# Performance work log

Hardware: AMD Instinct MI355X
Metric: run time of the kernel (lower is better)

The kernel has to match this reference:

```python
import jax, jax.numpy as jnp
import numpy as np

N = 50000      # num_nodes
E = 800000     # edges (before self loops)
IN = 64        # in_dim
H = 128        # hidden_node_dim
DH = 256       # decoder_and_message_hidden_dim
L = 3          # propagation_steps


def _lin(key, fan_in, fan_out):
    s = 1.0 / np.sqrt(fan_in)
    return jax.random.uniform(key, (fan_in, fan_out), jnp.float32, -s, s)


def setup_inputs() -> dict:
    key = jax.random.key(0)
    ks = iter(jax.random.split(key, 40))
    x = jax.random.normal(next(ks), (N, IN), jnp.float32)
    edge_index = jax.random.randint(next(ks), (2, E), 0, N, jnp.int64)
    enc_W = _lin(next(ks), IN, H); enc_b = jnp.zeros((H,), jnp.float32)
    # message MLP: Linear(2H->DH) tanh, Linear(DH->DH) tanh, Linear(DH->H)
    msg_W0 = jnp.stack([_lin(next(ks), 2 * H, DH) for _ in range(L)])
    msg_b0 = jnp.zeros((L, DH), jnp.float32)
    msg_W1 = jnp.stack([_lin(next(ks), DH, DH) for _ in range(L)])
    msg_b1 = jnp.zeros((L, DH), jnp.float32)
    msg_W2 = jnp.stack([_lin(next(ks), DH, H) for _ in range(L)])
    msg_b2 = jnp.zeros((L, H), jnp.float32)
    # GRUCell params, torch layout [3H, H] chunks (r, z, n)
    gru_Wih = jnp.stack([_lin(next(ks), H, 3 * H).T for _ in range(L)])
    gru_Whh = jnp.stack([_lin(next(ks), H, 3 * H).T for _ in range(L)])
    gru_bih = jnp.zeros((L, 3 * H), jnp.float32)
    gru_bhh = jnp.zeros((L, 3 * H), jnp.float32)
    # decoder: Linear(H->DH) tanh, Linear(DH->DH) tanh, Linear(DH->1)
    dec_W0 = _lin(next(ks), H, DH); dec_b0 = jnp.zeros((DH,), jnp.float32)
    dec_W1 = _lin(next(ks), DH, DH); dec_b1 = jnp.zeros((DH,), jnp.float32)
    dec_W2 = _lin(next(ks), DH, 1); dec_b2 = jnp.zeros((1,), jnp.float32)
    return dict(x=x, edge_index=edge_index, enc_W=enc_W, enc_b=enc_b,
                msg_W0=msg_W0, msg_b0=msg_b0, msg_W1=msg_W1, msg_b1=msg_b1,
                msg_W2=msg_W2, msg_b2=msg_b2, gru_Wih=gru_Wih, gru_Whh=gru_Whh,
                gru_bih=gru_bih, gru_bhh=gru_bhh, dec_W0=dec_W0, dec_b0=dec_b0,
                dec_W1=dec_W1, dec_b1=dec_b1, dec_W2=dec_W2, dec_b2=dec_b2)


def reference(x, edge_index, enc_W, enc_b, msg_W0, msg_b0, msg_W1, msg_b1,
              msg_W2, msg_b2, gru_Wih, gru_Whh, gru_bih, gru_bhh,
              dec_W0, dec_b0, dec_W1, dec_b1, dec_W2, dec_b2):
    n = x.shape[0]
    # add self loops (PyG add_self_loops appends (v, v))
    loops = jnp.arange(n, dtype=edge_index.dtype)
    src = jnp.concatenate([edge_index[0], loops])  # j (source)
    dst = jnp.concatenate([edge_index[1], loops])  # i (target)
    counts = jax.ops.segment_sum(jnp.ones_like(dst, jnp.float32), dst, num_segments=n)
    h = jnp.tanh(x @ enc_W + enc_b)                # encoder [N, H]
    for l in range(L):
        # message: f([x_i || x_j]) per edge
        m = jnp.concatenate([h[dst], h[src]], axis=-1)            # [E+N, 2H]
        m = jnp.tanh(m @ msg_W0[l] + msg_b0[l])
        m = jnp.tanh(m @ msg_W1[l] + msg_b1[l])
        m = m @ msg_W2[l] + msg_b2[l]                              # [E+N, H]
        aggr = jax.ops.segment_sum(m, dst, num_segments=n) / counts[:, None]
        # GRUCell(input=aggr, hidden=h)
        gi = aggr @ gru_Wih[l].T + gru_bih[l]                      # [N, 3H]
        gh = h @ gru_Whh[l].T + gru_bhh[l]
        i_r, i_z, i_n = jnp.split(gi, 3, axis=-1)
        h_r, h_z, h_n = jnp.split(gh, 3, axis=-1)
        r = jax.nn.sigmoid(i_r + h_r)
        z = jax.nn.sigmoid(i_z + h_z)
        nn_ = jnp.tanh(i_n + r * h_n)
        h = (1.0 - z) * nn_ + z * h
    # decoder
    y = jnp.tanh(h @ dec_W0 + dec_b0)
    y = jnp.tanh(y @ dec_W1 + dec_b1)
    y = y @ dec_W2 + dec_b2                                        # [N, 1]
    return y.reshape(-1, n)[0]                                     # view(-1, N).squeeze(0)
```

## Files before the change

### kernel.cpp

```cpp
#include <hip/hip_runtime.h>

typedef __bf16 bf16x8 __attribute__((ext_vector_type(8)));
typedef float  f32x4  __attribute__((ext_vector_type(4)));

__device__ inline unsigned short f2bf(float f){
  __bf16 b = (__bf16)f;
  return __builtin_bit_cast(unsigned short, b);
}
__device__ inline unsigned int pack2bf(float lo, float hi){
  return (unsigned)f2bf(lo) | ((unsigned)f2bf(hi) << 16);
}
__device__ inline float tanh_fast(float x){
  float e = __builtin_amdgcn_exp2f(x * 2.8853900817779268f);
  return 1.0f - 2.0f * __builtin_amdgcn_rcpf(e + 1.0f);
}
__device__ inline float sigmoid_fast(float x){
  float e = __builtin_amdgcn_exp2f(x * -1.4426950408889634f);
  return __builtin_amdgcn_rcpf(1.0f + e);
}
__device__ inline float bflo(unsigned int u){ return __uint_as_float(u << 16); }
__device__ inline float bfhi(unsigned int u){ return __uint_as_float(u & 0xffff0000u); }

__global__ void k_count(const int* __restrict__ ei, int* __restrict__ cnt, int E){
  int e = blockIdx.x * 256 + threadIdx.x;
  if (e < E) atomicAdd(&cnt[ei[E + e]], 1);
}

__global__ __launch_bounds__(1024) void k_scan(const int* __restrict__ cnt, int* __restrict__ cursor, int N){
  __shared__ int partial[1024];
  int t = threadIdx.x;
  int chunk = (N + 1023) / 1024;
  int lo = t * chunk, hi = min(lo + chunk, N);
  int s = 0;
  for (int v = lo; v < hi; v++) s += cnt[v] + 1;
  partial[t] = s;
  __syncthreads();
  for (int off = 1; off < 1024; off <<= 1){
    int val = (t >= off) ? partial[t - off] : 0;
    __syncthreads();
    partial[t] += val;
    __syncthreads();
  }
  int base = (t == 0) ? 0 : partial[t - 1];
  for (int v = lo; v < hi; v++){ cursor[v] = base; base += cnt[v] + 1; }
}

__global__ void k_scatter(const int* __restrict__ ei, int* __restrict__ cursor,
                          int* __restrict__ srcS, int* __restrict__ dstS, int E, int N){
  int i = blockIdx.x * 256 + threadIdx.x;
  int Et = E + N;
  if (i >= Et) return;
  int s, d;
  if (i < E){ s = ei[i]; d = ei[E + i]; } else { s = d = i - E; }
  int pos = atomicAdd(&cursor[d], 1);
// ... 161 lines not shown
    }
    bf16x8 afA[4], afB[4];
    #pragma unroll
    for (int ct = 0; ct < 4; ct++){
      int r = c64 + ct * 16 + l15;
      afA[ct] = *(const bf16x8*)(wa + (size_t)r * 256 + koff);
      afB[ct] = *(const bf16x8*)(wb + (size_t)r * 256 + koff);
    }
    #pragma unroll
    for (int ct = 0; ct < 4; ct++)
      #pragma unroll
      for (int nt = 0; nt < 4; nt++){
        accA[ct][nt] = __builtin_amdgcn_mfma_f32_16x16x32_bf16(afA[ct], bfr[nt], accA[ct][nt], 0, 0, 0);
        accB[ct][nt] = __builtin_amdgcn_mfma_f32_16x16x32_bf16(afB[ct], bfr[nt], accB[ct][nt], 0, 0, 0);
      }
  }
  #pragma unroll
  for (int ct = 0; ct < 4; ct++){
    int c = c64 + ct * 16 + kg * 4;
    #pragma unroll
    for (int nt = 0; nt < 4; nt++){
      int node = n0 + nt * 16 + l15;
      if (node >= N) continue;
      f32x4 va = accA[ct][nt], vb = accB[ct][nt];
      uint2 oa, ob;
      oa.x = pack2bf(va[0], va[1]); oa.y = pack2bf(va[2], va[3]);
      ob.x = pack2bf(vb[0], vb[1]); ob.y = pack2bf(vb[2], vb[3]);
      *(uint2*)(A + (size_t)node * 256 + c) = oa;
      *(uint2*)(B + (size_t)node * 256 + c) = ob;
    }
  }
}

__global__ __launch_bounds__(256, 3) void k_edge(
        const int* __restrict__ srcS, const int* __restrict__ dstS,
        const unsigned short* __restrict__ Abuf, const unsigned short* __restrict__ Bbuf,
        const unsigned short* __restrict__ W1T, const unsigned short* __restrict__ W2T,
        const float* __restrict__ b1, const float* __restrict__ b2,
        float* __restrict__ aggr){
  __shared__ __align__(16) unsigned char smem[64 * 512];
  __shared__ __align__(16) unsigned char t1h[64 * 256];
  __shared__ int sIdx[64], dIdx[64];
  __shared__ int segStart[64];
  __shared__ int nsegS, endAllS;
  unsigned char* t0 = smem;
  int t = threadIdx.x;
  int e0 = blockIdx.x * 64;
  if (t < 64){ sIdx[t] = srcS[e0 + t]; dIdx[t] = dstS[e0 + t]; }
  __syncthreads();

  int chunk = t & 31, rbase = t >> 5;
  uint4 av[8], bv[8];
  #pragma unroll
  for (int p = 0; p < 8; p++){
    int row = p * 8 + rbase;
    int d = dIdx[row], s = sIdx[row];
    if (d >= 0){
      av[p] = *(const uint4*)(Abuf + (size_t)d * 256 + chunk * 8);
      bv[p] = *(const uint4*)(Bbuf + (size_t)s * 256 + chunk * 8);
    } else { av[p] = make_uint4(0,0,0,0); bv[p] = make_uint4(0,0,0,0); }
  }
  if (t < 64){
    int d = dIdx[t];
    bool valid = (d >= 0);
    bool flag  = valid && (t == 0 || dIdx[t - 1] != d);
    unsigned long long startMask = __ballot(flag);
    unsigned long long invMask   = __ballot(!valid);
    if (flag){
      int s = __popcll(startMask & ((1ull << t) - 1ull));
      segStart[s] = t;
    }
    if (t == 0){
      nsegS   = (int)__popcll(startMask);
      endAllS = 64 - (int)__popcll(invMask);
    }
  }

  {
    #pragma unroll
    for (int p = 0; p < 8; p++){
      int r = p * 8 + rbase;
      unsigned int o[4]; unsigned int ua, ub;
      ua = av[p].x; ub = bv[p].x;
      o[0] = pack2bf(tanh_fast(bflo(ua)+bflo(ub)), tanh_fast(bfhi(ua)+bfhi(ub)));
      ua = av[p].y; ub = bv[p].y;
      o[1] = pack2bf(tanh_fast(bflo(ua)+bflo(ub)), tanh_fast(bfhi(ua)+bfhi(ub)));
      ua = av[p].z; ub = bv[p].z;
      o[2] = pack2bf(tanh_fast(bflo(ua)+bflo(ub)), tanh_fast(bfhi(ua)+bfhi(ub)));
      ua = av[p].w; ub = bv[p].w;
      o[3] = pack2bf(tanh_fast(bflo(ua)+bflo(ub)), tanh_fast(bfhi(ua)+bfhi(ub)));
      *(uint4*)(t0 + r * 512 + ((chunk * 16) ^ ((r & 7) << 4))) = make_uint4(o[0],o[1],o[2],o[3]);
    }
  }
  __syncthreads();

  int wv = t >> 6, lane = t & 63, l15 = lane & 15, kg = lane >> 4;
  const unsigned char* w1b = (const unsigned char*)W1T;
  const unsigned char* w2b = (const unsigned char*)W2T;
  int hbase = wv * 32;

  f32x4 acc2[2][4];
  #pragma unroll
  for (int ht = 0; ht < 2; ht++){
    int hb_ = hbase + ht * 16 + kg * 4;
    float4 c4 = *(const float4*)(b2 + hb_);
    f32x4 binit = {c4.x, c4.y, c4.z, c4.w};
    #pragma unroll
    for (int b_ = 0; b_ < 4; b_++) acc2[ht][b_] = binit;
  }

  #pragma unroll
  for (int pass = 0; pass < 2; pass++){
    {
      f32x4 acc[2][4];
      int nbase = pass * 128 + wv * 32;
      #pragma unroll
      for (int nt = 0; nt < 2; nt++){
        int ng = nbase + nt * 16 + kg * 4;
        float4 c4 = *(const float4*)(b1 + ng);
        f32x4 binit = {c4.x, c4.y, c4.z, c4.w};
        #pragma unroll
        for (int b_ = 0; b_ < 4; b_++) acc[nt][b_] = binit;
      }
      #pragma unroll
      for (int ks = 0; ks < 8; ks++){
        int koff = ks * 64 + kg * 16;
        bf16x8 afr[2], bfr[4];
        #pragma unroll
        for (int nt = 0; nt < 2; nt++)
          afr[nt] = *(const bf16x8*)(w1b + (size_t)(nbase + nt * 16 + l15) * 512 + koff);
        #pragma unroll
        for (int et = 0; et < 4; et++){
          int row = et * 16 + l15;
          bfr[et] = *(const bf16x8*)(t0 + row * 512 + (koff ^ ((row & 7) << 4)));
        }
        #pragma unroll
        for (int nt = 0; nt < 2; nt++)
          #pragma unroll
          for (int et = 0; et < 4; et++)
            acc[nt][et] = __builtin_amdgcn_mfma_f32_16x16x32_bf16(afr[nt], bfr[et], acc[nt][et], 0, 0, 0);
      }
      #pragma unroll
      for (int nt = 0; nt < 2; nt++){
        int nl2 = (wv * 32 + nt * 16 + kg * 4) * 2;
        #pragma unroll
        for (int et = 0; et < 4; et++){
          int edge = et * 16 + l15;
          f32x4 v = acc[nt][et];
          unsigned int p0 = pack2bf(tanh_fast(v[0]), tanh_fast(v[1]));
          unsigned int p1 = pack2bf(tanh_fast(v[2]), tanh_fast(v[3]));
          *(uint2*)(t1h + edge * 256 + (nl2 ^ ((edge & 7) << 4))) = make_uint2(p0, p1);
        }
      }
    }
    __syncthreads();

    #pragma unroll
    for (int ks = 0; ks < 4; ks++){
      int koff  = ks * 64 + kg * 16;
      int wkoff = pass * 256 + koff;
      bf16x8 afr[2], bfr[4];
      #pragma unroll
      for (int ht = 0; ht < 2; ht++)
        afr[ht] = *(const bf16x8*)(w2b + (size_t)(hbase + ht * 16 + l15) * 512 + wkoff);
      #pragma unroll
      for (int et = 0; et < 4; et++){
        int row = et * 16 + l15;
        bfr[et] = *(const bf16x8*)(t1h + row * 256 + (koff ^ ((row & 7) << 4)));
      }
      #pragma unroll
      for (int ht = 0; ht < 2; ht++)
        #pragma unroll
        for (int et = 0; et < 4; et++)
          acc2[ht][et] = __builtin_amdgcn_mfma_f32_16x16x32_bf16(afr[ht], bfr[et], acc2[ht][et], 0, 0, 0);
    }
    __syncthreads();
  }

  {
    #pragma unroll
    for (int ht = 0; ht < 2; ht++){
      int hb_ = hbase + ht * 16 + kg * 4;
      int cch = hb_ >> 2;
      #pragma unroll
      for (int et = 0; et < 4; et++){
        int edge = et * 16 + l15;
        f32x4 v = acc2[ht][et];
        float4 o; o.x = v[0]; o.y = v[1]; o.z = v[2]; o.w = v[3];
        *(float4*)(smem + edge * 512 + ((cch ^ (edge & 7)) << 4)) = o;
      }
    }
  }
  __syncthreads();

  {
    int c = t & 31, sstr = t >> 5;
    int nseg = nsegS, endAll = endAllS;
    for (int s = sstr; s < nseg; s += 8){
      int st = segStart[s];
      int en = (s + 1 < nseg) ? segStart[s + 1] : endAll;
      int d  = dIdx[st];
      float4 sum; sum.x = sum.y = sum.z = sum.w = 0.f;
      for (int e = st; e < en; e++){
        float4 v = *(const float4*)(smem + e * 512 + ((c ^ (e & 7)) << 4));
        sum.x += v.x; sum.y += v.y; sum.z += v.z; sum.w += v.w;
      }
      float* base = aggr + (size_t)d * 128 + c * 4;
      atomicAdd(base + 0, sum.x);
      atomicAdd(base + 1, sum.y);
      atomicAdd(base + 2, sum.z);
      atomicAdd(base + 3, sum.w);
    }
  }
}

__global__ __launch_bounds__(256) void k_gru(const float* __restrict__ aggr, const int* __restrict__ cnt,
    float* __restrict__ h, unsigned short* __restrict__ hb,
    const unsigned short* __restrict__ Wcat, const float* __restrict__ brz,
    const float* __restrict__ bin, const float* __restrict__ bhn, int N){
  __shared__ __align__(16) unsigned char u[64 * 512];
  __shared__ __align__(16) unsigned char hf[64 * 512];
  int n0 = blockIdx.x * 64, t = threadIdx.x;
  {
    int row = t >> 2, node = n0 + row;
    int q4 = t & 3;
    bool isA = q4 < 2;
    float inv = 0.f;
    if (isA && node < N) inv = __builtin_amdgcn_rcpf((float)(cnt[node] + 1));
    #pragma unroll
    for (int p = 0; p < 8; p++){
      int ch = q4 * 8 + p;
      unsigned int o[4] = {0,0,0,0};
      if (node < N){
        if (isA){
          const float* s = aggr + (size_t)node * 128 + ch * 8;
          float4 a = *(const float4*)s, b = *(const float4*)(s + 4);
          a.x *= inv; a.y *= inv; a.z *= inv; a.w *= inv;
          b.x *= inv; b.y *= inv; b.z *= inv; b.w *= inv;
          o[0] = pack2bf(a.x, a.y); o[1] = pack2bf(a.z, a.w);
          o[2] = pack2bf(b.x, b.y); o[3] = pack2bf(b.z, b.w);
        } else {
          const float* s = h + (size_t)node * 128 + (ch - 16) * 8;
          float4 a = *(const float4*)s, b = *(const float4*)(s + 4);
          o[0] = pack2bf(a.x, a.y); o[1] = pack2bf(a.z, a.w);
          o[2] = pack2bf(b.x, b.y); o[3] = pack2bf(b.z, b.w);
// ... 213 lines not shown
    if (part == 0 && (n0 + node) < N) out[n0 + node] = p + db2[0];
  }
}

extern "C" void kernel_launch(void* const* d_in, const int* in_sizes, int n_in,
                              void* d_out, int out_size, void* d_ws, size_t ws_size,
                              hipStream_t stream){
  const float* x     = (const float*)d_in[0];
  const int*   ei    = (const int*)  d_in[1];
  const float* encW  = (const float*)d_in[2];
  const float* encb  = (const float*)d_in[3];
  const float* msgW0 = (const float*)d_in[4];
  const float* msgb0 = (const float*)d_in[5];
  const float* msgW1 = (const float*)d_in[6];
  const float* msgb1 = (const float*)d_in[7];
  const float* msgW2 = (const float*)d_in[8];
  const float* msgb2 = (const float*)d_in[9];
  const float* gWih  = (const float*)d_in[10];
  const float* gWhh  = (const float*)d_in[11];
  const float* gbih  = (const float*)d_in[12];
  const float* gbhh  = (const float*)d_in[13];
  const float* dW0   = (const float*)d_in[14];
  const float* db0   = (const float*)d_in[15];
  const float* dW1   = (const float*)d_in[16];
  const float* db1   = (const float*)d_in[17];
  const float* dW2   = (const float*)d_in[18];
  const float* db2   = (const float*)d_in[19];
  int N = in_sizes[0] / 64;
  int E = in_sizes[1] / 2;
  float* out = (float*)d_out;

  int Et = E + N;
  int EtPad = (Et + 63) & ~63;

  char* ws = (char*)d_ws;
  size_t off = 0;
  auto alloc = [&](size_t bytes)->void*{
    void* p = ws + off; off += (bytes + 255) & ~(size_t)255; return p;
  };
  float*          h      = (float*)         alloc((size_t)N * 128 * 4);
  unsigned short* hbuf   = (unsigned short*)alloc((size_t)N * 128 * 2);
  unsigned short* Abuf   = (unsigned short*)alloc((size_t)N * 256 * 2);
  unsigned short* Bbuf   = (unsigned short*)alloc((size_t)N * 256 * 2);
  float*          aggr   = (float*)         alloc((size_t)N * 128 * 4);
  int*            cnt    = (int*)           alloc((size_t)N * 4);
  int*            cursor = (int*)           alloc((size_t)N * 4);
  int*            srcS   = (int*)           alloc((size_t)EtPad * 4);
  int*            dstS   = (int*)           alloc((size_t)EtPad * 4);
  unsigned short* W1T    = (unsigned short*)alloc((size_t)3 * 65536 * 2);
  unsigned short* W2T    = (unsigned short*)alloc((size_t)3 * 32768 * 2);
  unsigned short* W0T    = (unsigned short*)alloc((size_t)3 * 65536 * 2);
  unsigned short* Wcat   = (unsigned short*)alloc((size_t)3 * 98304 * 2);
  unsigned short* encWT  = (unsigned short*)alloc((size_t)8192 * 2);
  unsigned short* dW0T   = (unsigned short*)alloc((size_t)32768 * 2);
  unsigned short* dW1T   = (unsigned short*)alloc((size_t)65536 * 2);
  float*          brz    = (float*)         alloc((size_t)768 * 4);
  float*          binb   = (float*)         alloc((size_t)384 * 4);
  float*          bhnb   = (float*)         alloc((size_t)384 * 4);
  (void)ws_size; (void)n_in; (void)out_size;

  hipMemsetAsync(cnt, 0, (size_t)N * 4, stream);
  hipMemsetAsync(dstS, 0xFF, (size_t)EtPad * 4, stream);
  k_count<<<(E + 255) / 256, 256, 0, stream>>>(ei, cnt, E);
  k_scan<<<1, 1024, 0, stream>>>(cnt, cursor, N);
  k_scatter<<<(Et + 255) / 256, 256, 0, stream>>>(ei, cursor, srcS, dstS, E, N);
  k_wprep<<<(3 * 65536 + 3 * 32768 + 255) / 256, 256, 0, stream>>>(msgW1, msgW2, W1T, W2T);
  k_wprep2<<<(3 * 65536 + 255) / 256, 256, 0, stream>>>(msgW0, W0T);
  k_wprep3<<<(3 * 98304 + 255) / 256, 256, 0, stream>>>(gWih, gWhh, Wcat);
  k_wprep4<<<(108032 + 255) / 256, 256, 0, stream>>>(encW, dW0, dW1, gbih, gbhh,
                                                     encWT, dW0T, dW1T, brz, binb, bhnb);

  int nb64 = (N + 63) / 64;
  k_enc<<<nb64, 256, 0, stream>>>(x, encWT, encb, h, hbuf, N);

  int eb = EtPad / 64;
  for (int l = 0; l < 3; l++){
    k_ab<<<nb64, 256, 0, stream>>>(hbuf, W0T + (size_t)l * 65536, msgb0 + (size_t)l * 256,
                                   Abuf, Bbuf, N);
    hipMemsetAsync(aggr, 0, (size_t)N * 128 * 4, stream);
    k_edge<<<eb, 256, 0, stream>>>(srcS, dstS, Abuf, Bbuf,
        W1T + (size_t)l * 65536, W2T + (size_t)l * 32768,
        msgb1 + (size_t)l * 256, msgb2 + (size_t)l * 128,
        aggr);
    k_gru<<<nb64, 256, 0, stream>>>(aggr, cnt, h, hbuf,
        Wcat + (size_t)l * 98304, brz + (size_t)l * 256,
        binb + (size_t)l * 128, bhnb + (size_t)l * 128, N);
  }
  k_dec<<<nb64, 256, 0, stream>>>(hbuf, dW0T, db0, dW1T, db1, dW2, db2, out, N);
}
```

Baseline: 1.573 ms.

## Make edge kernel persistent with double-buffered gather prefetch across tiles

Converts k_edge from one 64-edge tile per block into a persistent kernel with 768 blocks, each walking a contiguous range of tiles. The next tile's indices and its A/B row gathers are issued before the current tile's MFMA work, so gather latency overlaps compute. It also swaps __syncthreads for a barrier that waits only on LDS counters, leaving the prefetched global loads in flight. Block-to-range mapping is interleaved by blockIdx&7, and the extra live registers for prefetch may reduce occupancy.

```diff
diff --git a/kernel.cpp b/kernel.cpp
--- a/kernel.cpp
+++ b/kernel.cpp
@@ -20,6 +20,11 @@
 }
 __device__ inline float bflo(unsigned int u){ return __uint_as_float(u << 16); }
 __device__ inline float bfhi(unsigned int u){ return __uint_as_float(u & 0xffff0000u); }
+
+__device__ __forceinline__ void bar_nodrain(){
+  asm volatile("s_waitcnt lgkmcnt(0)" ::: "memory");
+  __builtin_amdgcn_s_barrier();
+}
 
 __global__ void k_count(const int* __restrict__ ei, int* __restrict__ cnt, int E){
   int e = blockIdx.x * 256 + threadIdx.x;
@@ -252,46 +257,72 @@
         const unsigned short* __restrict__ Abuf, const unsigned short* __restrict__ Bbuf,
         const unsigned short* __restrict__ W1T, const unsigned short* __restrict__ W2T,
         const float* __restrict__ b1, const float* __restrict__ b2,
-        float* __restrict__ aggr){
+        float* __restrict__ aggr, int nT){
   __shared__ __align__(16) unsigned char smem[64 * 512];
   __shared__ __align__(16) unsigned char t1h[64 * 256];
-  __shared__ int sIdx[64], dIdx[64];
+  __shared__ int sI[2][64], dI[2][64];
   __shared__ int segStart[64];
   __shared__ int nsegS, endAllS;
   unsigned char* t0 = smem;
   int t = threadIdx.x;
-  int e0 = blockIdx.x * 64;
-  if (t < 64){ sIdx[t] = srcS[e0 + t]; dIdx[t] = dstS[e0 + t]; }
+
+  int nb   = gridDim.x;
+  int rb   = (blockIdx.x & 7) * (nb >> 3) + (blockIdx.x >> 3);
+  int cpb  = (nT + nb - 1) / nb;
+  int tstart = rb * cpb;
+  int tend   = min(tstart + cpb, nT);
+  if (tstart >= tend) return;
+
+  int chunk = t & 31, rbase = t >> 5;
+  int wv = t >> 6, lane = t & 63, l15 = lane & 15, kg = lane >> 4;
+  const unsigned char* w1b = (const unsigned char*)W1T;
+  const unsigned char* w2b = (const unsigned char*)W2T;
+  int hbase = wv * 32;
+
+  uint4 av[8], bv[8];
+  auto issue = [&](int buf){
+    #pragma unroll
+    for (int p = 0; p < 8; p++){
+      int row = p * 8 + rbase;
+      int d = dI[buf][row], s = sI[buf][row];
+      if (d >= 0){
+        av[p] = *(const uint4*)(Abuf + (size_t)d * 256 + chunk * 8);
+        bv[p] = *(const uint4*)(Bbuf + (size_t)s * 256 + chunk * 8);
+      } else { av[p] = make_uint4(0,0,0,0); bv[p] = make_uint4(0,0,0,0); }
+    }
+  };
+
+  if (t < 64){
+    int e = tstart * 64 + t;
+    sI[0][t] = srcS[e]; dI[0][t] = dstS[e];
+  }
   __syncthreads();
-
-  int chunk = t & 31, rbase = t >> 5;
-  uint4 av[8], bv[8];
-  #pragma unroll
-  for (int p = 0; p < 8; p++){
-    int row = p * 8 + rbase;
-    int d = dIdx[row], s = sIdx[row];
-    if (d >= 0){
-      av[p] = *(const uint4*)(Abuf + (size_t)d * 256 + chunk * 8);
-      bv[p] = *(const uint4*)(Bbuf + (size_t)s * 256 + chunk * 8);
-    } else { av[p] = make_uint4(0,0,0,0); bv[p] = make_uint4(0,0,0,0); }
-  }
-  if (t < 64){
-    int d = dIdx[t];
-    bool valid = (d >= 0);
-    bool flag  = valid && (t == 0 || dIdx[t - 1] != d);
-    unsigned long long startMask = __ballot(flag);
-    unsigned long long invMask   = __ballot(!valid);
-    if (flag){
-      int s = __popcll(startMask & ((1ull << t) - 1ull));
-      segStart[s] = t;
-    }
-    if (t == 0){
-      nsegS   = (int)__popcll(startMask);
-      endAllS = 64 - (int)__popcll(invMask);
-    }
-  }
-
-  {
+  issue(0);
+  int par = 0;
+
+  for (int ti = tstart; ti < tend; ++ti){
+    bool hasNext = (ti + 1 < tend);
+    int sReg = 0, dReg = -1;
+    if (hasNext && t < 64){
+      int e = (ti + 1) * 64 + t;
+      sReg = srcS[e]; dReg = dstS[e];
+    }
+    if (t < 64){
+      int d = dI[par][t];
+      bool valid = (d >= 0);
+      bool flag  = valid && (t == 0 || dI[par][t - 1] != d);
+      unsigned long long startMask = __ballot(flag);
+      unsigned long long invMask   = __ballot(!valid);
+      if (flag){
+        int s = __popcll(startMask & ((1ull << t) - 1ull));
+        segStart[s] = t;
+      }
+      if (t == 0){
+        nsegS   = (int)__popcll(startMask);
+        endAllS = 64 - (int)__popcll(invMask);
+      }
+    }
+
     #pragma unroll
     for (int p = 0; p < 8; p++){
       int r = p * 8 + rbase;
@@ -306,93 +337,89 @@
       o[3] = pack2bf(tanh_fast(bflo(ua)+bflo(ub)), tanh_fast(bfhi(ua)+bfhi(ub)));
       *(uint4*)(t0 + r * 512 + ((chunk * 16) ^ ((r & 7) << 4))) = make_uint4(o[0],o[1],o[2],o[3]);
     }
-  }
-  __syncthreads();
-
-  int wv = t >> 6, lane = t & 63, l15 = lane & 15, kg = lane >> 4;
-  const unsigned char* w1b = (const unsigned char*)W1T;
-  const unsigned char* w2b = (const unsigned char*)W2T;
-  int hbase = wv * 32;
-
-  f32x4 acc2[2][4];
-  #pragma unroll
-  for (int ht = 0; ht < 2; ht++){
-    int hb_ = hbase + ht * 16 + kg * 4;
-    float4 c4 = *(const float4*)(b2 + hb_);
-    f32x4 binit = {c4.x, c4.y, c4.z, c4.w};
-    #pragma unroll
-    for (int b_ = 0; b_ < 4; b_++) acc2[ht][b_] = binit;
-  }
-
-  #pragma unroll
-  for (int pass = 0; pass < 2; pass++){
-    {
-      f32x4 acc[2][4];
-      int nbase = pass * 128 + wv * 32;
-      #pragma unroll
-      for (int nt = 0; nt < 2; nt++){
-        int ng = nbase + nt * 16 + kg * 4;
-        float4 c4 = *(const float4*)(b1 + ng);
-        f32x4 binit = {c4.x, c4.y, c4.z, c4.w};
-        #pragma unroll
-        for (int b_ = 0; b_ < 4; b_++) acc[nt][b_] = binit;
-      }
-      #pragma unroll
-      for (int ks = 0; ks < 8; ks++){
-        int koff = ks * 64 + kg * 16;
+    if (hasNext && t < 64){ sI[par ^ 1][t] = sReg; dI[par ^ 1][t] = dReg; }
+    bar_nodrain();
+
+    if (hasNext) issue(par ^ 1);
+
+    f32x4 acc2[2][4];
+    #pragma unroll
+    for (int ht = 0; ht < 2; ht++){
+      int hb_ = hbase + ht * 16 + kg * 4;
+      float4 c4 = *(const float4*)(b2 + hb_);
+      f32x4 binit = {c4.x, c4.y, c4.z, c4.w};
+      #pragma unroll
+      for (int b_ = 0; b_ < 4; b_++) acc2[ht][b_] = binit;
+    }
+
+    #pragma unroll
+    for (int pass = 0; pass < 2; pass++){
+      {
+        f32x4 acc[2][4];
+        int nbase = pass * 128 + wv * 32;
+        #pragma unroll
+        for (int nt = 0; nt < 2; nt++){
+          int ng = nbase + nt * 16 + kg * 4;
+          float4 c4 = *(const float4*)(b1 + ng);
+          f32x4 binit = {c4.x, c4.y, c4.z, c4.w};
+          #pragma unroll
+          for (int b_ = 0; b_ < 4; b_++) acc[nt][b_] = binit;
+        }
+        #pragma unroll
+        for (int ks = 0; ks < 8; ks++){
+          int koff = ks * 64 + kg * 16;
+          bf16x8 afr[2], bfr[4];
+          #pragma unroll
+          for (int nt = 0; nt < 2; nt++)
+            afr[nt] = *(const bf16x8*)(w1b + (size_t)(nbase + nt * 16 + l15) * 512 + koff);
+          #pragma unroll
+          for (int et = 0; et < 4; et++){
+            int row = et * 16 + l15;
+            bfr[et] = *(const bf16x8*)(t0 + row * 512 + (koff ^ ((row & 7) << 4)));
+          }
+          #pragma unroll
+          for (int nt = 0; nt < 2; nt++)
+            #pragma unroll
+            for (int et = 0; et < 4; et++)
+              acc[nt][et] = __builtin_amdgcn_mfma_f32_16x16x32_bf16(afr[nt], bfr[et], acc[nt][et], 0, 0, 0);
+        }
+        #pragma unroll
+        for (int nt = 0; nt < 2; nt++){
+          int nl2 = (wv * 32 + nt * 16 + kg * 4) * 2;
+          #pragma unroll
+          for (int et = 0; et < 4; et++){
+            int edge = et * 16 + l15;
+            f32x4 v = acc[nt][et];
+            unsigned int p0 = pack2bf(tanh_fast(v[0]), tanh_fast(v[1]));
+            unsigned int p1 = pack2bf(tanh_fast(v[2]), tanh_fast(v[3]));
+            *(uint2*)(t1h + edge * 256 + (nl2 ^ ((edge & 7) << 4))) = make_uint2(p0, p1);
+          }
+        }
+      }
+      bar_nodrain();
+
+      #pragma unroll
+      for (int ks = 0; ks < 4; ks++){
+        int koff  = ks * 64 + kg * 16;
+        int wkoff = pass * 256 + koff;
         bf16x8 afr[2], bfr[4];
         #pragma unroll
-        for (int nt = 0; nt < 2; nt++)
-          afr[nt] = *(const bf16x8*)(w1b + (size_t)(nbase + nt * 16 + l15) * 512 + koff);
+        for (int ht = 0; ht < 2; ht++)
+          afr[ht] = *(const bf16x8*)(w2b + (size_t)(hbase + ht * 16 + l15) * 512 + wkoff);
         #pragma unroll
         for (int et = 0; et < 4; et++){
           int row = et * 16 + l15;
-          bfr[et] = *(const bf16x8*)(t0 + row * 512 + (koff ^ ((row & 7) << 4)));
+          bfr[et] = *(const bf16x8*)(t1h + row * 256 + (koff ^ ((row & 7) << 4)));
         }
         #pragma unroll
-        for (int nt = 0; nt < 2; nt++)
+        for (int ht = 0; ht < 2; ht++)
           #pragma unroll
           for (int et = 0; et < 4; et++)
-            acc[nt][et] = __builtin_amdgcn_mfma_f32_16x16x32_bf16(afr[nt], bfr[et], acc[nt][et], 0, 0, 0);
-      }
-      #pragma unroll
-      for (int nt = 0; nt < 2; nt++){
-        int nl2 = (wv * 32 + nt * 16 + kg * 4) * 2;
-        #pragma unroll
-        for (int et = 0; et < 4; et++){
-          int edge = et * 16 + l15;
-          f32x4 v = acc[nt][et];
-          unsigned int p0 = pack2bf(tanh_fast(v[0]), tanh_fast(v[1]));
-          unsigned int p1 = pack2bf(tanh_fast(v[2]), tanh_fast(v[3]));
-          *(uint2*)(t1h + edge * 256 + (nl2 ^ ((edge & 7) << 4))) = make_uint2(p0, p1);
-        }
-      }
-    }
-    __syncthreads();
-
-    #pragma unroll
-    for (int ks = 0; ks < 4; ks++){
-      int koff  = ks * 64 + kg * 16;
-      int wkoff = pass * 256 + koff;
-      bf16x8 afr[2], bfr[4];
-      #pragma unroll
-      for (int ht = 0; ht < 2; ht++)
-        afr[ht] = *(const bf16x8*)(w2b + (size_t)(hbase + ht * 16 + l15) * 512 + wkoff);
-      #pragma unroll
-      for (int et = 0; et < 4; et++){
-        int row = et * 16 + l15;
-        bfr[et] = *(const bf16x8*)(t1h + row * 256 + (koff ^ ((row & 7) << 4)));
-      }
-      #pragma unroll
-      for (int ht = 0; ht < 2; ht++)
-        #pragma unroll
-        for (int et = 0; et < 4; et++)
-          acc2[ht][et] = __builtin_amdgcn_mfma_f32_16x16x32_bf16(afr[ht], bfr[et], acc2[ht][et], 0, 0, 0);
-    }
-    __syncthreads();
-  }
-
-  {
+            acc2[ht][et] = __builtin_amdgcn_mfma_f32_16x16x32_bf16(afr[ht], bfr[et], acc2[ht][et], 0, 0, 0);
+      }
+      bar_nodrain();
+    }
+
     #pragma unroll
     for (int ht = 0; ht < 2; ht++){
       int hb_ = hbase + ht * 16 + kg * 4;
@@ -405,27 +432,29 @@
         *(float4*)(smem + edge * 512 + ((cch ^ (edge & 7)) << 4)) = o;
       }
     }
-  }
-  __syncthreads();
-
-  {
-    int c = t & 31, sstr = t >> 5;
-    int nseg = nsegS, endAll = endAllS;
-    for (int s = sstr; s < nseg; s += 8){
-      int st = segStart[s];
-      int en = (s + 1 < nseg) ? segStart[s + 1] : endAll;
-      int d  = dIdx[st];
-      float4 sum; sum.x = sum.y = sum.z = sum.w = 0.f;
-      for (int e = st; e < en; e++){
-        float4 v = *(const float4*)(smem + e * 512 + ((c ^ (e & 7)) << 4));
-        sum.x += v.x; sum.y += v.y; sum.z += v.z; sum.w += v.w;
-      }
-      float* base = aggr + (size_t)d * 128 + c * 4;
-      atomicAdd(base + 0, sum.x);
-      atomicAdd(base + 1, sum.y);
-      atomicAdd(base + 2, sum.z);
-      atomicAdd(base + 3, sum.w);
-    }
+    bar_nodrain();
+
+    {
+      int c = t & 31, sstr = t >> 5;
+      int nseg = nsegS, endAll = endAllS;
+      for (int s = sstr; s < nseg; s += 8){
+        int st = segStart[s];
+        int en = (s + 1 < nseg) ? segStart[s + 1] : endAll;
+        int d  = dI[par][st];
+        float4 sum; sum.x = sum.y = sum.z = sum.w = 0.f;
+        for (int e = st; e < en; e++){
+          float4 v = *(const float4*)(smem + e * 512 + ((c ^ (e & 7)) << 4));
+          sum.x += v.x; sum.y += v.y; sum.z += v.z; sum.w += v.w;
+        }
+        float* base = aggr + (size_t)d * 128 + c * 4;
+        atomicAdd(base + 0, sum.x);
+        atomicAdd(base + 1, sum.y);
+        atomicAdd(base + 2, sum.z);
+        atomicAdd(base + 3, sum.w);
+      }
+    }
+    bar_nodrain();
+    par ^= 1;
   }
 }
 
@@ -705,6 +734,7 @@
 
   int Et = E + N;
   int EtPad = (Et + 63) & ~63;
+  int nT = EtPad / 64;
 
   char* ws = (char*)d_ws;
   size_t off = 0;
@@ -746,15 +776,15 @@
   int nb64 = (N + 63) / 64;
   k_enc<<<nb64, 256, 0, stream>>>(x, encWT, encb, h, hbuf, N);
 
-  int eb = EtPad / 64;
+  const int EDGE_BLOCKS = 768;
   for (int l = 0; l < 3; l++){
     k_ab<<<nb64, 256, 0, stream>>>(hbuf, W0T + (size_t)l * 65536, msgb0 + (size_t)l * 256,
                                    Abuf, Bbuf, N);
     hipMemsetAsync(aggr, 0, (size_t)N * 128 * 4, stream);
-    k_edge<<<eb, 256, 0, stream>>>(srcS, dstS, Abuf, Bbuf,
+    k_edge<<<EDGE_BLOCKS, 256, 0, stream>>>(srcS, dstS, Abuf, Bbuf,
         W1T + (size_t)l * 65536, W2T + (size_t)l * 32768,
         msgb1 + (size_t)l * 256, msgb2 + (size_t)l * 128,
-        aggr);
+        aggr, nT);
     k_gru<<<nb64, 256, 0, stream>>>(aggr, cnt, h, hbuf,
         Wcat + (size_t)l * 98304, brz + (size_t)l * 256,
         binb + (size_t)l * 128, bhnb + (size_t)l * 128, N);
```

Measured after the change: 2.174 ms. 38.2% more time.

## Make edge-MLP kernel wave-independent with 16 edges per wave

Applied to the files above, without the earlier changes.

Restructures the edge kernel so each wavefront handles its own 16 edges end to end, with private LDS tiles. Block-wide __syncthreads barriers are replaced by per-wave LDS waitcnt fences, and segment detection moves to shuffles and ballots. Each wave now walks all 256/128 output columns, so every weight fragment is reused across only 16 edges instead of 64. That raises global and L2 weight traffic per edge in exchange for removing barriers and the cross-wave dependencies. Relying only on s_waitcnt for intra-wave LDS ordering also assumes the whole wavefront executes in lockstep.

```diff
diff --git a/kernel.cpp b/kernel.cpp
--- a/kernel.cpp
+++ b/kernel.cpp
@@ -20,6 +20,10 @@
 }
 __device__ inline float bflo(unsigned int u){ return __uint_as_float(u << 16); }
 __device__ inline float bfhi(unsigned int u){ return __uint_as_float(u & 0xffff0000u); }
+
+__device__ __forceinline__ void fence_lds(){
+  asm volatile("s_waitcnt lgkmcnt(0)" ::: "memory");
+}
 
 __global__ void k_count(const int* __restrict__ ei, int* __restrict__ cnt, int E){
   int e = blockIdx.x * 256 + threadIdx.x;
@@ -253,171 +257,140 @@
         const unsigned short* __restrict__ W1T, const unsigned short* __restrict__ W2T,
         const float* __restrict__ b1, const float* __restrict__ b2,
         float* __restrict__ aggr){
-  __shared__ __align__(16) unsigned char smem[64 * 512];
-  __shared__ __align__(16) unsigned char t1h[64 * 256];
-  __shared__ int sIdx[64], dIdx[64];
-  __shared__ int segStart[64];
-  __shared__ int nsegS, endAllS;
-  unsigned char* t0 = smem;
+  __shared__ __align__(16) unsigned char t0s[4 * 8192];
+  __shared__ __align__(16) unsigned char t1s[4 * 4096];
+  __shared__ int segStartS[4][16];
+  __shared__ int segDstS[4][16];
   int t = threadIdx.x;
-  int e0 = blockIdx.x * 64;
-  if (t < 64){ sIdx[t] = srcS[e0 + t]; dIdx[t] = dstS[e0 + t]; }
-  __syncthreads();
-
-  int chunk = t & 31, rbase = t >> 5;
+  int wv = t >> 6, lane = t & 63, l15 = lane & 15, kg = lane >> 4;
+  unsigned char* t0w = t0s + wv * 8192;
+  unsigned char* t1w = t1s + wv * 4096;
+
+  int e0 = (blockIdx.x * 4 + wv) * 16;
+  int sv = 0, dv = -1;
+  if (lane < 16){ sv = srcS[e0 + lane]; dv = dstS[e0 + lane]; }
+  int myEdge = lane >> 2;
+  int c2 = lane & 3;
+  int dE = __shfl(dv, myEdge);
+  int sE = __shfl(sv, myEdge);
+
   uint4 av[8], bv[8];
   #pragma unroll
   for (int p = 0; p < 8; p++){
-    int row = p * 8 + rbase;
-    int d = dIdx[row], s = sIdx[row];
-    if (d >= 0){
-      av[p] = *(const uint4*)(Abuf + (size_t)d * 256 + chunk * 8);
-      bv[p] = *(const uint4*)(Bbuf + (size_t)s * 256 + chunk * 8);
+    int ch = c2 * 8 + p;
+    if (dE >= 0){
+      av[p] = *(const uint4*)(Abuf + (size_t)dE * 256 + ch * 8);
+      bv[p] = *(const uint4*)(Bbuf + (size_t)sE * 256 + ch * 8);
     } else { av[p] = make_uint4(0,0,0,0); bv[p] = make_uint4(0,0,0,0); }
   }
-  if (t < 64){
-    int d = dIdx[t];
-    bool valid = (d >= 0);
-    bool flag  = valid && (t == 0 || dIdx[t - 1] != d);
-    unsigned long long startMask = __ballot(flag);
-    unsigned long long invMask   = __ballot(!valid);
-    if (flag){
-      int s = __popcll(startMask & ((1ull << t) - 1ull));
-      segStart[s] = t;
-    }
-    if (t == 0){
-      nsegS   = (int)__popcll(startMask);
-      endAllS = 64 - (int)__popcll(invMask);
-    }
-  }
-
-  {
-    #pragma unroll
-    for (int p = 0; p < 8; p++){
-      int r = p * 8 + rbase;
-      unsigned int o[4]; unsigned int ua, ub;
-      ua = av[p].x; ub = bv[p].x;
-      o[0] = pack2bf(tanh_fast(bflo(ua)+bflo(ub)), tanh_fast(bfhi(ua)+bfhi(ub)));
-      ua = av[p].y; ub = bv[p].y;
-      o[1] = pack2bf(tanh_fast(bflo(ua)+bflo(ub)), tanh_fast(bfhi(ua)+bfhi(ub)));
-      ua = av[p].z; ub = bv[p].z;
-      o[2] = pack2bf(tanh_fast(bflo(ua)+bflo(ub)), tanh_fast(bfhi(ua)+bfhi(ub)));
-      ua = av[p].w; ub = bv[p].w;
-      o[3] = pack2bf(tanh_fast(bflo(ua)+bflo(ub)), tanh_fast(bfhi(ua)+bfhi(ub)));
-      *(uint4*)(t0 + r * 512 + ((chunk * 16) ^ ((r & 7) << 4))) = make_uint4(o[0],o[1],o[2],o[3]);
-    }
-  }
-  __syncthreads();
-
-  int wv = t >> 6, lane = t & 63, l15 = lane & 15, kg = lane >> 4;
+
+  int prevd = __shfl(dv, (lane == 0) ? 0 : (lane - 1));
+  bool valid16 = (lane < 16) && (dv >= 0);
+  bool flag = valid16 && (lane == 0 || prevd != dv);
+  unsigned long long sm  = __ballot(flag);
+  unsigned long long ivm = __ballot((lane < 16) && (dv < 0));
+  int nseg   = (int)__popcll(sm);
+  int endAll = 16 - (int)__popcll(ivm);
+  if (flag){
+    int s = (int)__popcll(sm & ((1ull << lane) - 1ull));
+    segStartS[wv][s] = lane;
+    segDstS[wv][s]   = dv;
+  }
+
+  #pragma unroll
+  for (int p = 0; p < 8; p++){
+    int ch = c2 * 8 + p;
+    unsigned int o[4]; unsigned int ua, ub;
+    ua = av[p].x; ub = bv[p].x;
+    o[0] = pack2bf(tanh_fast(bflo(ua)+bflo(ub)), tanh_fast(bfhi(ua)+bfhi(ub)));
+    ua = av[p].y; ub = bv[p].y;
+    o[1] = pack2bf(tanh_fast(bflo(ua)+bflo(ub)), tanh_fast(bfhi(ua)+bfhi(ub)));
+    ua = av[p].z; ub = bv[p].z;
+    o[2] = pack2bf(tanh_fast(bflo(ua)+bflo(ub)), tanh_fast(bfhi(ua)+bfhi(ub)));
+    ua = av[p].w; ub = bv[p].w;
+    o[3] = pack2bf(tanh_fast(bflo(ua)+bflo(ub)), tanh_fast(bfhi(ua)+bfhi(ub)));
+    *(uint4*)(t0w + myEdge * 512 + ((ch * 16) ^ ((myEdge & 7) << 4))) = make_uint4(o[0],o[1],o[2],o[3]);
+  }
+  fence_lds();
+
   const unsigned char* w1b = (const unsigned char*)W1T;
   const unsigned char* w2b = (const unsigned char*)W2T;
-  int hbase = wv * 32;
-
-  f32x4 acc2[2][4];
-  #pragma unroll
-  for (int ht = 0; ht < 2; ht++){
-    int hb_ = hbase + ht * 16 + kg * 4;
+
+  f32x4 acc2[8];
+  #pragma unroll
+  for (int ht = 0; ht < 8; ht++){
+    int hb_ = ht * 16 + kg * 4;
     float4 c4 = *(const float4*)(b2 + hb_);
     f32x4 binit = {c4.x, c4.y, c4.z, c4.w};
-    #pragma unroll
-    for (int b_ = 0; b_ < 4; b_++) acc2[ht][b_] = binit;
+    acc2[ht] = binit;
   }
 
   #pragma unroll
   for (int pass = 0; pass < 2; pass++){
     {
-      f32x4 acc[2][4];
-      int nbase = pass * 128 + wv * 32;
-      #pragma unroll
-      for (int nt = 0; nt < 2; nt++){
+      f32x4 acc[8];
+      int nbase = pass * 128;
+      #pragma unroll
+      for (int nt = 0; nt < 8; nt++){
         int ng = nbase + nt * 16 + kg * 4;
         float4 c4 = *(const float4*)(b1 + ng);
         f32x4 binit = {c4.x, c4.y, c4.z, c4.w};
-        #pragma unroll
-        for (int b_ = 0; b_ < 4; b_++) acc[nt][b_] = binit;
+        acc[nt] = binit;
       }
       #pragma unroll
       for (int ks = 0; ks < 8; ks++){
         int koff = ks * 64 + kg * 16;
-        bf16x8 afr[2], bfr[4];
+        bf16x8 bfr = *(const bf16x8*)(t0w + l15 * 512 + (koff ^ ((l15 & 7) << 4)));
         #pragma unroll
-        for (int nt = 0; nt < 2; nt++)
-          afr[nt] = *(const bf16x8*)(w1b + (size_t)(nbase + nt * 16 + l15) * 512 + koff);
-        #pragma unroll
-        for (int et = 0; et < 4; et++){
-          int row = et * 16 + l15;
-          bfr[et] = *(const bf16x8*)(t0 + row * 512 + (koff ^ ((row & 7) << 4)));
+        for (int nt = 0; nt < 8; nt++){
+          bf16x8 afr = *(const bf16x8*)(w1b + (size_t)(nbase + nt * 16 + l15) * 512 + koff);
+          acc[nt] = __builtin_amdgcn_mfma_f32_16x16x32_bf16(afr, bfr, acc[nt], 0, 0, 0);
         }
-        #pragma unroll
-        for (int nt = 0; nt < 2; nt++)
-          #pragma unroll
-          for (int et = 0; et < 4; et++)
-            acc[nt][et] = __builtin_amdgcn_mfma_f32_16x16x32_bf16(afr[nt], bfr[et], acc[nt][et], 0, 0, 0);
-      }
-      #pragma unroll
-      for (int nt = 0; nt < 2; nt++){
-        int nl2 = (wv * 32 + nt * 16 + kg * 4) * 2;
-        #pragma unroll
-        for (int et = 0; et < 4; et++){
-          int edge = et * 16 + l15;
-          f32x4 v = acc[nt][et];
-          unsigned int p0 = pack2bf(tanh_fast(v[0]), tanh_fast(v[1]));
-          unsigned int p1 = pack2bf(tanh_fast(v[2]), tanh_fast(v[3]));
-          *(uint2*)(t1h + edge * 256 + (nl2 ^ ((edge & 7) << 4))) = make_uint2(p0, p1);
-        }
-      }
-    }
-    __syncthreads();
+      }
+      #pragma unroll
+      for (int nt = 0; nt < 8; nt++){
+        int nl2 = (nt * 16 + kg * 4) * 2;
+        f32x4 v = acc[nt];
+        unsigned int p0 = pack2bf(tanh_fast(v[0]), tanh_fast(v[1]));
+        unsigned int p1 = pack2bf(tanh_fast(v[2]), tanh_fast(v[3]));
+        *(uint2*)(t1w + l15 * 256 + (nl2 ^ ((l15 & 7) << 4))) = make_uint2(p0, p1);
+      }
+    }
+    fence_lds();
 
     #pragma unroll
     for (int ks = 0; ks < 4; ks++){
       int koff  = ks * 64 + kg * 16;
       int wkoff = pass * 256 + koff;
-      bf16x8 afr[2], bfr[4];
-      #pragma unroll
-      for (int ht = 0; ht < 2; ht++)
-        afr[ht] = *(const bf16x8*)(w2b + (size_t)(hbase + ht * 16 + l15) * 512 + wkoff);
-      #pragma unroll
-      for (int et = 0; et < 4; et++){
-        int row = et * 16 + l15;
-        bfr[et] = *(const bf16x8*)(t1h + row * 256 + (koff ^ ((row & 7) << 4)));
-      }
-      #pragma unroll
-      for (int ht = 0; ht < 2; ht++)
-        #pragma unroll
-        for (int et = 0; et < 4; et++)
-          acc2[ht][et] = __builtin_amdgcn_mfma_f32_16x16x32_bf16(afr[ht], bfr[et], acc2[ht][et], 0, 0, 0);
-    }
-    __syncthreads();
-  }
+      bf16x8 bfr = *(const bf16x8*)(t1w + l15 * 256 + (koff ^ ((l15 & 7) << 4)));
+      #pragma unroll
+      for (int ht = 0; ht < 8; ht++){
+        bf16x8 afr = *(const bf16x8*)(w2b + (size_t)(ht * 16 + l15) * 512 + wkoff);
+        acc2[ht] = __builtin_amdgcn_mfma_f32_16x16x32_bf16(afr, bfr, acc2[ht], 0, 0, 0);
+      }
+    }
+    fence_lds();
+  }
+
+  #pragma unroll
+  for (int ht = 0; ht < 8; ht++){
+    int hb_ = ht * 16 + kg * 4;
+    int cch = hb_ >> 2;
+    f32x4 v = acc2[ht];
+    float4 o; o.x = v[0]; o.y = v[1]; o.z = v[2]; o.w = v[3];
+    *(float4*)(t0w + l15 * 512 + ((cch ^ (l15 & 7)) << 4)) = o;
+  }
+  fence_lds();
 
   {
-    #pragma unroll
-    for (int ht = 0; ht < 2; ht++){
-      int hb_ = hbase + ht * 16 + kg * 4;
-      int cch = hb_ >> 2;
-      #pragma unroll
-      for (int et = 0; et < 4; et++){
-        int edge = et * 16 + l15;
-        f32x4 v = acc2[ht][et];
-        float4 o; o.x = v[0]; o.y = v[1]; o.z = v[2]; o.w = v[3];
-        *(float4*)(smem + edge * 512 + ((cch ^ (edge & 7)) << 4)) = o;
-      }
-    }
-  }
-  __syncthreads();
-
-  {
-    int c = t & 31, sstr = t >> 5;
-    int nseg = nsegS, endAll = endAllS;
-    for (int s = sstr; s < nseg; s += 8){
-      int st = segStart[s];
-      int en = (s + 1 < nseg) ? segStart[s + 1] : endAll;
-      int d  = dIdx[st];
+    int c = lane & 31, sstr = lane >> 5;
+    for (int s = sstr; s < nseg; s += 2){
+      int st = segStartS[wv][s];
+      int en = (s + 1 < nseg) ? segStartS[wv][s + 1] : endAll;
+      int d  = segDstS[wv][s];
       float4 sum; sum.x = sum.y = sum.z = sum.w = 0.f;
       for (int e = st; e < en; e++){
-        float4 v = *(const float4*)(smem + e * 512 + ((c ^ (e & 7)) << 4));
+        float4 v = *(const float4*)(t0w + e * 512 + ((c ^ (e & 7)) << 4));
         sum.x += v.x; sum.y += v.y; sum.z += v.z; sum.w += v.w;
       }
       float* base = aggr + (size_t)d * 128 + c * 4;
```

Result: slower. 4.389 ms (+179.0%).

## Shrink edge-kernel LDS, compute segments via wave shuffles, raise occupancy

Applied to the files above, without the earlier changes.

The edge MLP kernel now stages the second hidden layer in four quarter passes of 64 columns instead of two halves of 128. This cuts the intermediate LDS buffer to 8KB and the total to 40KB, allowing four blocks per CU instead of three. Edge indices and segment boundaries are computed per wave with shuffles and ballots instead of shared arrays, removing one barrier. Barriers now wait only on LDS counters, not global memory, so the gathers can stay in flight. The cost is more barriers per block and smaller per-pass MFMA tiles with less weight reuse.

```diff
diff --git a/kernel.cpp b/kernel.cpp
--- a/kernel.cpp
+++ b/kernel.cpp
@@ -20,6 +20,16 @@
 }
 __device__ inline float bflo(unsigned int u){ return __uint_as_float(u << 16); }
 __device__ inline float bfhi(unsigned int u){ return __uint_as_float(u & 0xffff0000u); }
+
+__device__ __forceinline__ void bar_nodrain(){
+  asm volatile("s_waitcnt lgkmcnt(0)" ::: "memory");
+  __builtin_amdgcn_s_barrier();
+}
+
+__device__ inline int nthbit(unsigned long long m, int n){
+  for (int k = 0; k < n; k++) m &= m - 1;
+  return m ? (int)__builtin_ctzll(m) : 0;
+}
 
 __global__ void k_count(const int* __restrict__ ei, int* __restrict__ cnt, int E){
   int e = blockIdx.x * 256 + threadIdx.x;
@@ -247,69 +257,67 @@
   }
 }
 
-__global__ __launch_bounds__(256, 3) void k_edge(
+__global__ __launch_bounds__(256, 4) void k_edge(
         const int* __restrict__ srcS, const int* __restrict__ dstS,
         const unsigned short* __restrict__ Abuf, const unsigned short* __restrict__ Bbuf,
         const unsigned short* __restrict__ W1T, const unsigned short* __restrict__ W2T,
         const float* __restrict__ b1, const float* __restrict__ b2,
         float* __restrict__ aggr){
-  __shared__ __align__(16) unsigned char smem[64 * 512];
-  __shared__ __align__(16) unsigned char t1h[64 * 256];
-  __shared__ int sIdx[64], dIdx[64];
-  __shared__ int segStart[64];
-  __shared__ int nsegS, endAllS;
-  unsigned char* t0 = smem;
+  __shared__ __align__(16) unsigned char lds[40960];
+  unsigned char* t0  = lds;
+  unsigned char* t1q = lds + 32768;
   int t = threadIdx.x;
+  int wv = t >> 6, lane = t & 63, l15 = lane & 15, kg = lane >> 4;
   int e0 = blockIdx.x * 64;
-  if (t < 64){ sIdx[t] = srcS[e0 + t]; dIdx[t] = dstS[e0 + t]; }
-  __syncthreads();
-
-  int chunk = t & 31, rbase = t >> 5;
+
+  int sv = srcS[e0 + lane];
+  int dv = dstS[e0 + lane];
+
+  int chunk = lane & 31;
+  int rbase = wv * 2 + (lane >> 5);
   uint4 av[8], bv[8];
   #pragma unroll
   for (int p = 0; p < 8; p++){
     int row = p * 8 + rbase;
-    int d = dIdx[row], s = sIdx[row];
+    int d = __shfl(dv, row), s = __shfl(sv, row);
     if (d >= 0){
       av[p] = *(const uint4*)(Abuf + (size_t)d * 256 + chunk * 8);
       bv[p] = *(const uint4*)(Bbuf + (size_t)s * 256 + chunk * 8);
     } else { av[p] = make_uint4(0,0,0,0); bv[p] = make_uint4(0,0,0,0); }
   }
-  if (t < 64){
-    int d = dIdx[t];
-    bool valid = (d >= 0);
-    bool flag  = valid && (t == 0 || dIdx[t - 1] != d);
-    unsigned long long startMask = __ballot(flag);
-    unsigned long long invMask   = __ballot(!valid);
-    if (flag){
-      int s = __popcll(startMask & ((1ull << t) - 1ull));
-      segStart[s] = t;
-    }
-    if (t == 0){
-      nsegS   = (int)__popcll(startMask);
-      endAllS = 64 - (int)__popcll(invMask);
-    }
-  }
-
+
+  int prevd = __shfl(dv, (lane == 0) ? 0 : (lane - 1));
+  bool valid = (dv >= 0);
+  bool flag  = valid && (lane == 0 || prevd != dv);
+  unsigned long long sm  = __ballot(flag);
+  unsigned long long ivm = __ballot(!valid);
+  int nseg   = (int)__popcll(sm);
+  int endAll = 64 - (int)__popcll(ivm);
+
+  int segSt, segEn, segD;
   {
-    #pragma unroll
-    for (int p = 0; p < 8; p++){
-      int r = p * 8 + rbase;
-      unsigned int o[4]; unsigned int ua, ub;
-      ua = av[p].x; ub = bv[p].x;
-      o[0] = pack2bf(tanh_fast(bflo(ua)+bflo(ub)), tanh_fast(bfhi(ua)+bfhi(ub)));
-      ua = av[p].y; ub = bv[p].y;
-      o[1] = pack2bf(tanh_fast(bflo(ua)+bflo(ub)), tanh_fast(bfhi(ua)+bfhi(ub)));
-      ua = av[p].z; ub = bv[p].z;
-      o[2] = pack2bf(tanh_fast(bflo(ua)+bflo(ub)), tanh_fast(bfhi(ua)+bfhi(ub)));
-      ua = av[p].w; ub = bv[p].w;
-      o[3] = pack2bf(tanh_fast(bflo(ua)+bflo(ub)), tanh_fast(bfhi(ua)+bfhi(ub)));
-      *(uint4*)(t0 + r * 512 + ((chunk * 16) ^ ((r & 7) << 4))) = make_uint4(o[0],o[1],o[2],o[3]);
-    }
-  }
-  __syncthreads();
-
-  int wv = t >> 6, lane = t & 63, l15 = lane & 15, kg = lane >> 4;
+    int st_ = nthbit(sm, lane);
+    int en_ = (lane + 1 < nseg) ? nthbit(sm, lane + 1) : endAll;
+    segSt = st_; segEn = en_;
+    segD  = __shfl(dv, st_);
+  }
+
+  #pragma unroll
+  for (int p = 0; p < 8; p++){
+    int r = p * 8 + rbase;
+    unsigned int o[4]; unsigned int ua, ub;
+    ua = av[p].x; ub = bv[p].x;
+    o[0] = pack2bf(tanh_fast(bflo(ua)+bflo(ub)), tanh_fast(bfhi(ua)+bfhi(ub)));
+    ua = av[p].y; ub = bv[p].y;
+    o[1] = pack2bf(tanh_fast(bflo(ua)+bflo(ub)), tanh_fast(bfhi(ua)+bfhi(ub)));
+    ua = av[p].z; ub = bv[p].z;
+    o[2] = pack2bf(tanh_fast(bflo(ua)+bflo(ub)), tanh_fast(bfhi(ua)+bfhi(ub)));
+    ua = av[p].w; ub = bv[p].w;
+    o[3] = pack2bf(tanh_fast(bflo(ua)+bflo(ub)), tanh_fast(bfhi(ua)+bfhi(ub)));
+    *(uint4*)(t0 + r * 512 + ((chunk * 16) ^ ((r & 7) << 4))) = make_uint4(o[0],o[1],o[2],o[3]);
+  }
+  bar_nodrain();
+
   const unsigned char* w1b = (const unsigned char*)W1T;
   const unsigned char* w2b = (const unsigned char*)W2T;
   int hbase = wv * 32;
@@ -325,55 +333,47 @@
   }
 
   #pragma unroll
-  for (int pass = 0; pass < 2; pass++){
+  for (int pass = 0; pass < 4; pass++){
     {
-      f32x4 acc[2][4];
-      int nbase = pass * 128 + wv * 32;
-      #pragma unroll
-      for (int nt = 0; nt < 2; nt++){
-        int ng = nbase + nt * 16 + kg * 4;
+      int nbase = pass * 64 + wv * 16;
+      f32x4 acc[4];
+      {
+        int ng = nbase + kg * 4;
         float4 c4 = *(const float4*)(b1 + ng);
         f32x4 binit = {c4.x, c4.y, c4.z, c4.w};
         #pragma unroll
-        for (int b_ = 0; b_ < 4; b_++) acc[nt][b_] = binit;
+        for (int b_ = 0; b_ < 4; b_++) acc[b_] = binit;
       }
       #pragma unroll
       for (int ks = 0; ks < 8; ks++){
         int koff = ks * 64 + kg * 16;
-        bf16x8 afr[2], bfr[4];
-        #pragma unroll
-        for (int nt = 0; nt < 2; nt++)
-          afr[nt] = *(const bf16x8*)(w1b + (size_t)(nbase + nt * 16 + l15) * 512 + koff);
+        bf16x8 afr = *(const bf16x8*)(w1b + (size_t)(nbase + l15) * 512 + koff);
+        bf16x8 bfr[4];
         #pragma unroll
         for (int et = 0; et < 4; et++){
           int row = et * 16 + l15;
           bfr[et] = *(const bf16x8*)(t0 + row * 512 + (koff ^ ((row & 7) << 4)));
         }
         #pragma unroll
-        for (int nt = 0; nt < 2; nt++)
-          #pragma unroll
-          for (int et = 0; et < 4; et++)
-            acc[nt][et] = __builtin_amdgcn_mfma_f32_16x16x32_bf16(afr[nt], bfr[et], acc[nt][et], 0, 0, 0);
-      }
-      #pragma unroll
-      for (int nt = 0; nt < 2; nt++){
-        int nl2 = (wv * 32 + nt * 16 + kg * 4) * 2;
-        #pragma unroll
-        for (int et = 0; et < 4; et++){
-          int edge = et * 16 + l15;
-          f32x4 v = acc[nt][et];
-          unsigned int p0 = pack2bf(tanh_fast(v[0]), tanh_fast(v[1]));
-          unsigned int p1 = pack2bf(tanh_fast(v[2]), tanh_fast(v[3]));
-          *(uint2*)(t1h + edge * 256 + (nl2 ^ ((edge & 7) << 4))) = make_uint2(p0, p1);
-        }
-      }
-    }
-    __syncthreads();
-
-    #pragma unroll
-    for (int ks = 0; ks < 4; ks++){
+        for (int et = 0; et < 4; et++)
+          acc[et] = __builtin_amdgcn_mfma_f32_16x16x32_bf16(afr, bfr[et], acc[et], 0, 0, 0);
+      }
+      int nl2 = (wv * 16 + kg * 4) * 2;
+      #pragma unroll
+      for (int et = 0; et < 4; et++){
+        int edge = et * 16 + l15;
+        f32x4 v = acc[et];
+        unsigned int p0 = pack2bf(tanh_fast(v[0]), tanh_fast(v[1]));
+        unsigned int p1 = pack2bf(tanh_fast(v[2]), tanh_fast(v[3]));
+        *(uint2*)(t1q + edge * 128 + (nl2 ^ ((edge & 7) << 4))) = make_uint2(p0, p1);
+      }
+    }
+    bar_nodrain();
+
+    #pragma unroll
+    for (int ks = 0; ks < 2; ks++){
       int koff  = ks * 64 + kg * 16;
-      int wkoff = pass * 256 + koff;
+      int wkoff = pass * 128 + koff;
       bf16x8 afr[2], bfr[4];
       #pragma unroll
       for (int ht = 0; ht < 2; ht++)
@@ -381,7 +381,7 @@
       #pragma unroll
       for (int et = 0; et < 4; et++){
         int row = et * 16 + l15;
-        bfr[et] = *(const bf16x8*)(t1h + row * 256 + (koff ^ ((row & 7) << 4)));
+        bfr[et] = *(const bf16x8*)(t1q + row * 128 + (koff ^ ((row & 7) << 4)));
       }
       #pragma unroll
       for (int ht = 0; ht < 2; ht++)
@@ -389,42 +389,44 @@
         for (int et = 0; et < 4; et++)
           acc2[ht][et] = __builtin_amdgcn_mfma_f32_16x16x32_bf16(afr[ht], bfr[et], acc2[ht][et], 0, 0, 0);
     }
-    __syncthreads();
-  }
+    bar_nodrain();
+  }
+
+  #pragma unroll
+  for (int ht = 0; ht < 2; ht++){
+    int hb_ = hbase + ht * 16 + kg * 4;
+    int cch = hb_ >> 2;
+    #pragma unroll
+    for (int et = 0; et < 4; et++){
+      int edge = et * 16 + l15;
+      f32x4 v = acc2[ht][et];
+      float4 o; o.x = v[0]; o.y = v[1]; o.z = v[2]; o.w = v[3];
+      *(float4*)(t0 + edge * 512 + ((cch ^ (edge & 7)) << 4)) = o;
+    }
+  }
+  bar_nodrain();
 
   {
-    #pragma unroll
-    for (int ht = 0; ht < 2; ht++){
-      int hb_ = hbase + ht * 16 + kg * 4;
-      int cch = hb_ >> 2;
-      #pragma unroll
-      for (int et = 0; et < 4; et++){
-        int edge = et * 16 + l15;
-        f32x4 v = acc2[ht][et];
-        float4 o; o.x = v[0]; o.y = v[1]; o.z = v[2]; o.w = v[3];
-        *(float4*)(smem + edge * 512 + ((cch ^ (edge & 7)) << 4)) = o;
-      }
-    }
-  }
-  __syncthreads();
-
-  {
-    int c = t & 31, sstr = t >> 5;
-    int nseg = nsegS, endAll = endAllS;
-    for (int s = sstr; s < nseg; s += 8){
-      int st = segStart[s];
-      int en = (s + 1 < nseg) ? segStart[s + 1] : endAll;
-      int d  = dIdx[st];
-      float4 sum; sum.x = sum.y = sum.z = sum.w = 0.f;
-      for (int e = st; e < en; e++){
-        float4 v = *(const float4*)(smem + e * 512 + ((c ^ (e & 7)) << 4));
-        sum.x += v.x; sum.y += v.y; sum.z += v.z; sum.w += v.w;
-      }
-      float* base = aggr + (size_t)d * 128 + c * 4;
-      atomicAdd(base + 0, sum.x);
-      atomicAdd(base + 1, sum.y);
-      atomicAdd(base + 2, sum.z);
-      atomicAdd(base + 3, sum.w);
+    int c = lane & 31;
+    int sstr = wv * 2 + (lane >> 5);
+    #pragma unroll
+    for (int s0 = 0; s0 < 8; s0++){
+      int s = sstr + s0 * 8;
+      int st = __shfl(segSt, s);
+      int en = __shfl(segEn, s);
+      int d  = __shfl(segD,  s);
+      if (s < nseg){
+        float4 sum; sum.x = sum.y = sum.z = sum.w = 0.f;
+        for (int e = st; e < en; e++){
+          float4 v = *(const float4*)(t0 + e * 512 + ((c ^ (e & 7)) << 4));
+          sum.x += v.x; sum.y += v.y; sum.z += v.z; sum.w += v.w;
+        }
+        float* base = aggr + (size_t)d * 128 + c * 4;
+        atomicAdd(base + 0, sum.x);
+        atomicAdd(base + 1, sum.y);
+        atomicAdd(base + 2, sum.z);
+        atomicAdd(base + 3, sum.w);
+      }
     }
   }
 }
```

Result: faster. 1.527 ms (median of 2 runs) (-3.0%).
